# Kernel tuning notes

Measured on AMD Instinct MI355X. Metric: run time of the kernel, lower is better.

The kernel has to match this reference:

```python
import jax, jax.numpy as jnp
import numpy as np

N, T, D, H = 64, 1024, 512, 512

def setup_inputs() -> dict:
    key = jax.random.key(0)
    k1, k2, k3, k4 = jax.random.split(key, 4)
    x = jax.random.normal(k1, (N, T, D), dtype=jnp.float32)
    h0 = jax.random.normal(k2, (N, H), dtype=jnp.float32)
    Wx = jax.random.normal(k3, (D, 4 * H), dtype=jnp.float32) / jnp.sqrt(jnp.float32(D))
    Wh = jax.random.normal(k4, (H, 4 * H), dtype=jnp.float32) / jnp.sqrt(jnp.float32(H))
    b = jnp.zeros((4 * H,), dtype=jnp.float32)
    return {"x": x, "h0": h0, "Wx": Wx, "Wh": Wh, "b": b}

def reference(x, h0, Wx, Wh, b):
    Hd = h0.shape[1]
    c0 = jnp.zeros_like(h0)
    # Input projection for all timesteps at once (same math as per-step x@Wx).
    xw = jnp.einsum('ntd,dk->ntk', x, Wx) + b  # [N, T, 4H]

    def step(carry, xw_t):
        h, c = carry
        a = xw_t + h @ Wh  # [N, 4H]
        i = jax.nn.sigmoid(a[:, 0 * Hd:1 * Hd])
        f = jax.nn.sigmoid(a[:, 1 * Hd:2 * Hd])
        o = jax.nn.sigmoid(a[:, 2 * Hd:3 * Hd])
        g = jnp.tanh(a[:, 3 * Hd:4 * Hd])
        c_next = f * c + i * g
        h_next = o * jnp.tanh(c_next)
        return (h_next, c_next), h_next

    _, hs = jax.lax.scan(step, (h0, c0), jnp.swapaxes(xw, 0, 1))  # hs: [T, N, H]
    return jnp.swapaxes(hs, 0, 1)  # [N, T, H]
```

## Files before the change

kernel.cpp:

```cpp
#include <hip/hip_runtime.h>

typedef _Float16 f16;
typedef _Float16 f16x2 __attribute__((ext_vector_type(2)));
typedef _Float16 f16x8 __attribute__((ext_vector_type(8)));
typedef float f32x4 __attribute__((ext_vector_type(4)));
typedef unsigned int u32;
typedef u32 u32x4 __attribute__((ext_vector_type(4)));

#define OFF_WCAT  67108864L
#define OFF_BP    71303168L
#define OFF_H32   71311360L

constexpr int AS = 536;

__global__ void prep_kernel(const float* __restrict__ x, const float* __restrict__ h0,
                            const float* __restrict__ Wx, const float* __restrict__ Wh,
                            const float* __restrict__ b,
                            f16* __restrict__ x_h, f16* __restrict__ Wcat,
                            float* __restrict__ b_p, u32* __restrict__ h32)
{
    const int tid = blockIdx.x * blockDim.x + threadIdx.x;
    if (tid < 4194304) {
        const float4* src = (const float4*)x;
        float4 a = src[2*tid], c = src[2*tid + 1];
        f16x8 v;
        v[0]=(f16)a.x; v[1]=(f16)a.y; v[2]=(f16)a.z; v[3]=(f16)a.w;
        v[4]=(f16)c.x; v[5]=(f16)c.y; v[6]=(f16)c.z; v[7]=(f16)c.w;
        *(f16x8*)(x_h + (long)tid*8) = v;
    }
    if (tid < 2097152) {
        int q = tid >> 10, k = tid & 1023;
        int u = q >> 2, g = q & 3;
        float v = (k < 512) ? Wx[(long)k*2048 + g*512 + u]
                            : Wh[(long)(k-512)*2048 + g*512 + u];
        Wcat[tid] = (f16)v;
    }
    if (tid < 32768) {
        union { f16 h; unsigned short s; } cv; cv.h = (f16)h0[tid];
        h32[tid]         = (u32)cv.s;
        h32[32768 + tid] = 0xFFFF0000u;
    }
    if (tid < 2048)  b_p[tid] = b[(tid & 3)*512 + (tid >> 2)];
}


__device__ __forceinline__ void ld16_coh(const u32* p, u32x4& a, u32x4& b,
                                         u32x4& c, u32x4& d)
{
    asm volatile("global_load_dwordx4 %0, %4, off sc0 sc1\n\t"
                 "global_load_dwordx4 %1, %5, off sc0 sc1\n\t"
                 "global_load_dwordx4 %2, %6, off sc0 sc1\n\t"
                 "global_load_dwordx4 %3, %7, off sc0 sc1\n\t"
                 "s_waitcnt vmcnt(0)"
                 : "=&v"(a), "=&v"(b), "=&v"(c), "=&v"(d)
                 : "v"(p), "v"(p + 4), "v"(p + 8), "v"(p + 12)
                 : "memory");
}

__device__ __forceinline__ void st_w32(u32* p, unsigned v)
{
    asm volatile("global_store_dword %0, %1, off sc0 sc1" :: "v"(p), "v"(v) : "memory");
}

__device__ __forceinline__ void poll_stage(f16* __restrict__ Ah,
                                           const u32* __restrict__ wbase,
                                           unsigned tgt, int tid)
{
    const u32* p = wbase + tid * 16;
    u32x4 A, B, C, D;
    while (true) {
        ld16_coh(p, A, B, C, D);
        unsigned m;
        m  = (A.x>>16)^tgt; m |= (A.y>>16)^tgt; m |= (A.z>>16)^tgt; m |= (A.w>>16)^tgt;
        m |= (B.x>>16)^tgt; m |= (B.y>>16)^tgt; m |= (B.z>>16)^tgt; m |= (B.w>>16)^tgt;
        m |= (C.x>>16)^tgt; m |= (C.y>>16)^tgt; m |= (C.z>>16)^tgt; m |= (C.w>>16)^tgt;
        m |= (D.x>>16)^tgt; m |= (D.y>>16)^tgt; m |= (D.z>>16)^tgt; m |= (D.w>>16)^tgt;
        if (m == 0) break;
    }
    u32x4 lo, hi;
    lo.x = (A.x & 0xFFFFu) | (A.y << 16); lo.y = (A.z & 0xFFFFu) | (A.w << 16);
    lo.z = (B.x & 0xFFFFu) | (B.y << 16); lo.w = (B.z & 0xFFFFu) | (B.w << 16);
    hi.x = (C.x & 0xFFFFu) | (C.y << 16); hi.y = (C.z & 0xFFFFu) | (C.w << 16);
    hi.z = (D.x & 0xFFFFu) | (D.y << 16); hi.w = (D.z & 0xFFFFu) | (D.w << 16);
    const int row = tid >> 5;
    const int col = (tid & 31) * 16;
    u32* dst = (u32*)(Ah + row * AS + col);
    *(u32x4*)dst       = lo;
    *(u32x4*)(dst + 4) = hi;
}

__device__ __forceinline__ void mfma_quad(const f16* A, int aoff, const f16x8* wf,
                                          f32x4& a0, f32x4& a1, f32x4& a2, f32x4& a3)
{
    #pragma unroll
    for (int kk = 0; kk < 16; kk += 4) {
        f16x8 f0 = *(const f16x8*)(A + aoff + (kk+0) * 32);
        f16x8 f1 = *(const f16x8*)(A + aoff + (kk+1) * 32);
        f16x8 f2 = *(const f16x8*)(A + aoff + (kk+2) * 32);
        f16x8 f3 = *(const f16x8*)(A + aoff + (kk+3) * 32);
        a0 = __builtin_amdgcn_mfma_f32_16x16x32_f16(f0, wf[kk+0], a0, 0, 0, 0);
        a1 = __builtin_amdgcn_mfma_f32_16x16x32_f16(f1, wf[kk+1], a1, 0, 0, 0);
        a2 = __builtin_amdgcn_mfma_f32_16x16x32_f16(f2, wf[kk+2], a2, 0, 0, 0);
        a3 = __builtin_amdgcn_mfma_f32_16x16x32_f16(f3, wf[kk+3], a3, 0, 0, 0);
    }
}

__device__ __forceinline__ void bar_lds()
{
    asm volatile("s_waitcnt lgkmcnt(0)" ::: "memory");
    __builtin_amdgcn_s_barrier();
}

__global__ __launch_bounds__(256, 1) void lstm_kernel(
    const f16* __restrict__ x_h, const f16* __restrict__ Wcat,
    const float* __restrict__ b_p, u32* __restrict__ h32,
    float* __restrict__ out)
{
    __shared__ f16 Ax[8 * AS];
    __shared__ f16 Ah[8 * AS];
    __shared__ float epil[4 * 16 * 20];

    const int blk  = blockIdx.x;
    const int g    = blk & 7;
    const int wgl  = blk >> 3;
    const int n0   = g * 8;
    const int tid  = threadIdx.x;
    const int wave = tid >> 6;
    const int lane = tid & 63;
    const int c    = lane & 15;
    const int kg   = lane >> 4;
    const int ub   = wgl * 16 + wave * 4;
    const int q0   = ub * 4;

    f16x8 wfrag[32];
    {
        const f16* wp = Wcat + (long)(q0 + c) * 1024 + kg * 8;
        #pragma unroll
        for (int kk = 0; kk < 32; ++kk)
            wfrag[kk] = *(const f16x8*)(wp + kk * 32);
    }
    const float bias = b_p[q0 + c];

    const int aoff = (lane & 7) * AS + kg * 8;
    float* ep = epil + wave * 320;
    const int rb = lane >> 4;
    const int er = lane >> 2;
    const int eu = lane & 3;
    float cst = 0.f;
    int cur = 0;

    const int pr0 = tid >> 6, pch = tid & 63;
    const f16* xb0 = x_h + ((long)(n0 + pr0)     * 1024) * 512 + pch * 8;
    const f16* xb1 = x_h + ((long)(n0 + pr0 + 4) * 1024) * 512 + pch * 8;
    f16* axd0 = Ax + pr0       * AS + pch * 8;
    f16* axd1 = Ax + (pr0 + 4) * AS + pch * 8;

    u32* hb0 = h32 + n0 * 512;
    u32* hb1 = h32 + 32768 + n0 * 512;

    *(f16x8*)axd0 = *(const f16x8*)(xb0);
    *(f16x8*)axd1 = *(const f16x8*)(xb1);
    poll_stage(Ah, hb0, 0u, tid);
    __syncthreads();

    f32x4 a0 = {0.f,0.f,0.f,0.f}, a1 = {0.f,0.f,0.f,0.f};
    f32x4 a2 = {0.f,0.f,0.f,0.f}, a3 = {0.f,0.f,0.f,0.f};
    mfma_quad(Ax, aoff, wfrag, a0, a1, a2, a3);

    for (int t = 0; t < 1024; ++t) {
        f16x8 xv0, xv1;
        if (t < 1023) {
            xv0 = *(const f16x8*)(xb0 + (long)(t + 1) * 512);
            xv1 = *(const f16x8*)(xb1 + (long)(t + 1) * 512);
        }

        mfma_quad(Ah, aoff, wfrag + 16, a0, a1, a2, a3);

        #pragma unroll
        for (int j = 0; j < 4; ++j) {
            float av = ((a0[j] + a1[j]) + (a2[j] + a3[j])) + bias;
            ep[(rb * 4 + j) * 20 + c] = av;
        }

        const int nxt = cur ^ 1;
        if (lane < 32) {
            float4 g4 = *(const float4*)(ep + er * 20 + eu * 4);
            float iv = 1.f / (1.f + __expf(-g4.x));
            float fv = 1.f / (1.f + __expf(-g4.y));
            float ov = 1.f / (1.f + __expf(-g4.z));
            float gv = 2.f / (1.f + __expf(-2.f * g4.w)) - 1.f;
            float cn = fv * cst + iv * gv;
            cst = cn;
            float th = 2.f / (1.f + __expf(-2.f * cn)) - 1.f;
            float hval = ov * th;
            const int n = n0 + er;
            const int u = ub + eu;
            out[((long)n * 1024 + t) * 512 + u] = hval;
            if (t < 1023) {
                union { f16 h; unsigned short s; } cv; cv.h = (f16)hval;
                unsigned w = ((unsigned)(t + 1) << 16) | (unsigned)cv.s;
                st_w32((nxt ? hb1 : hb0) + (n - n0) * 512 + u, w);
            }
        }

        if (t < 1023) {
            bar_lds();

            *(f16x8*)axd0 = xv0;
            *(f16x8*)axd1 = xv1;
            bar_lds();

            a0 = (f32x4){0.f,0.f,0.f,0.f}; a1 = (f32x4){0.f,0.f,0.f,0.f};
            a2 = (f32x4){0.f,0.f,0.f,0.f}; a3 = (f32x4){0.f,0.f,0.f,0.f};
            mfma_quad(Ax, aoff, wfrag, a0, a1, a2, a3);

            poll_stage(Ah, nxt ? hb1 : hb0, (unsigned)(t + 1), tid);
            bar_lds();
            cur = nxt;
        }
    }
}

extern "C" void kernel_launch(void* const* d_in, const int* in_sizes, int n_in,
                              void* d_out, int out_size, void* d_ws, size_t ws_size,
                              hipStream_t stream)
{
    const float* x  = (const float*)d_in[0];
    const float* h0 = (const float*)d_in[1];
    const float* Wx = (const float*)d_in[2];
    const float* Wh = (const float*)d_in[3];
    const float* b  = (const float*)d_in[4];
    float* out = (float*)d_out;

    char* ws = (char*)d_ws;
    f16*   x_h  = (f16*)(ws);
    f16*   Wcat = (f16*)(ws + OFF_WCAT);
    float* b_p  = (float*)(ws + OFF_BP);
    u32*   h32  = (u32*)(ws + OFF_H32);

    prep_kernel<<<16384, 256, 0, stream>>>(x, h0, Wx, Wh, b, x_h, Wcat, b_p, h32);
    lstm_kernel<<<256, 256, 0, stream>>>(x_h, Wcat, b_p, h32, out);
}
```

Measured before the change: 2.239 ms.

## Offload input projection to producer waves via tagged ring buffer

Each workgroup grows to 512 threads. The extra four waves become producers that compute the x@Wx projection ahead of time into an 8-deep ring buffer of tagged fp16 values, and a progress array provides back-pressure. The recurrent waves now only do the h@Wh MFMAs per step and read the precomputed input term. The workgroup barrier is replaced with an LDS atomic counter barrier among the consumer waves. This takes the input GEMM and x loads off the serial critical path, but it adds polling traffic, fp16 rounding of the projection, and reliance on all blocks being co-resident.

```diff
diff --git a/kernel.cpp b/kernel.cpp
--- a/kernel.cpp
+++ b/kernel.cpp
@@ -1,7 +1,6 @@
 #include <hip/hip_runtime.h>
 
 typedef _Float16 f16;
-typedef _Float16 f16x2 __attribute__((ext_vector_type(2)));
 typedef _Float16 f16x8 __attribute__((ext_vector_type(8)));
 typedef float f32x4 __attribute__((ext_vector_type(4)));
 typedef unsigned int u32;
@@ -10,14 +9,18 @@
 #define OFF_WCAT  67108864L
 #define OFF_BP    71303168L
 #define OFF_H32   71311360L
+#define OFF_XW    71573504L
+#define OFF_PROG  75767808L
 
 constexpr int AS = 536;
+constexpr int XW_DEPTH = 8;
 
 __global__ void prep_kernel(const float* __restrict__ x, const float* __restrict__ h0,
                             const float* __restrict__ Wx, const float* __restrict__ Wh,
                             const float* __restrict__ b,
                             f16* __restrict__ x_h, f16* __restrict__ Wcat,
-                            float* __restrict__ b_p, u32* __restrict__ h32)
+                            float* __restrict__ b_p, u32* __restrict__ h32,
+                            u32* __restrict__ xw, u32* __restrict__ prog)
 {
     const int tid = blockIdx.x * blockDim.x + threadIdx.x;
     if (tid < 4194304) {
@@ -40,7 +43,9 @@
         h32[tid]         = (u32)cv.s;
         h32[32768 + tid] = 0xFFFF0000u;
     }
+    if (tid < 1048576) xw[tid] = 0u;
     if (tid < 2048)  b_p[tid] = b[(tid & 3)*512 + (tid >> 2)];
+    if (tid < 256)   prog[tid] = 0u;
 }
 
 
@@ -57,9 +62,29 @@
                  : "memory");
 }
 
+__device__ __forceinline__ unsigned ld_flag(const unsigned int* p)
+{
+    unsigned v;
+    asm volatile("global_load_dword %0, %1, off sc0 sc1\n\ts_waitcnt vmcnt(0)"
+                 : "=&v"(v) : "v"(p) : "memory");
+    return v;
+}
+
 __device__ __forceinline__ void st_w32(u32* p, unsigned v)
 {
     asm volatile("global_store_dword %0, %1, off sc0 sc1" :: "v"(p), "v"(v) : "memory");
+}
+
+__device__ __forceinline__ void ld4_nw(const u32* p, u32x4& v)
+{
+    asm volatile("global_load_dwordx4 %0, %1, off sc0 sc1"
+                 : "=&v"(v) : "v"(p) : "memory");
+}
+
+__device__ __forceinline__ float pay(u32 w)
+{
+    union { unsigned short s; f16 h; } u; u.s = (unsigned short)w;
+    return (float)u.h;
 }
 
 __device__ __forceinline__ void poll_stage(f16* __restrict__ Ah,
@@ -105,118 +130,162 @@
     }
 }
 
-__device__ __forceinline__ void bar_lds()
-{
+__device__ __forceinline__ void cbar(unsigned* cnt, unsigned& phase)
+{
+    phase += 4;
     asm volatile("s_waitcnt lgkmcnt(0)" ::: "memory");
-    __builtin_amdgcn_s_barrier();
-}
-
-__global__ __launch_bounds__(256, 1) void lstm_kernel(
+    if ((threadIdx.x & 63) == 0) atomicAdd(cnt, 1u);
+    while (*((volatile unsigned*)cnt) < phase) {}
+    asm volatile("" ::: "memory");
+}
+
+__global__ __launch_bounds__(512, 1) void lstm_kernel(
     const f16* __restrict__ x_h, const f16* __restrict__ Wcat,
     const float* __restrict__ b_p, u32* __restrict__ h32,
-    float* __restrict__ out)
-{
-    __shared__ f16 Ax[8 * AS];
+    u32* __restrict__ xw, u32* __restrict__ prog, float* __restrict__ out)
+{
     __shared__ f16 Ah[8 * AS];
     __shared__ float epil[4 * 16 * 20];
+    __shared__ unsigned rcnt;
 
     const int blk  = blockIdx.x;
-    const int g    = blk & 7;
-    const int wgl  = blk >> 3;
-    const int n0   = g * 8;
     const int tid  = threadIdx.x;
-    const int wave = tid >> 6;
     const int lane = tid & 63;
     const int c    = lane & 15;
     const int kg   = lane >> 4;
-    const int ub   = wgl * 16 + wave * 4;
-    const int q0   = ub * 4;
-
-    f16x8 wfrag[32];
-    {
-        const f16* wp = Wcat + (long)(q0 + c) * 1024 + kg * 8;
-        #pragma unroll
-        for (int kk = 0; kk < 32; ++kk)
-            wfrag[kk] = *(const f16x8*)(wp + kk * 32);
-    }
-    const float bias = b_p[q0 + c];
-
-    const int aoff = (lane & 7) * AS + kg * 8;
-    float* ep = epil + wave * 320;
-    const int rb = lane >> 4;
-    const int er = lane >> 2;
-    const int eu = lane & 3;
-    float cst = 0.f;
-    int cur = 0;
-
-    const int pr0 = tid >> 6, pch = tid & 63;
-    const f16* xb0 = x_h + ((long)(n0 + pr0)     * 1024) * 512 + pch * 8;
-    const f16* xb1 = x_h + ((long)(n0 + pr0 + 4) * 1024) * 512 + pch * 8;
-    f16* axd0 = Ax + pr0       * AS + pch * 8;
-    f16* axd1 = Ax + (pr0 + 4) * AS + pch * 8;
-
-    u32* hb0 = h32 + n0 * 512;
-    u32* hb1 = h32 + 32768 + n0 * 512;
-
-    *(f16x8*)axd0 = *(const f16x8*)(xb0);
-    *(f16x8*)axd1 = *(const f16x8*)(xb1);
-    poll_stage(Ah, hb0, 0u, tid);
+    const int rb   = kg;
+
+    if (tid == 0) rcnt = 0u;
     __syncthreads();
 
-    f32x4 a0 = {0.f,0.f,0.f,0.f}, a1 = {0.f,0.f,0.f,0.f};
-    f32x4 a2 = {0.f,0.f,0.f,0.f}, a3 = {0.f,0.f,0.f,0.f};
-    mfma_quad(Ax, aoff, wfrag, a0, a1, a2, a3);
-
-    for (int t = 0; t < 1024; ++t) {
-        f16x8 xv0, xv1;
-        if (t < 1023) {
-            xv0 = *(const f16x8*)(xb0 + (long)(t + 1) * 512);
-            xv1 = *(const f16x8*)(xb1 + (long)(t + 1) * 512);
+    if (tid < 256) {
+        const int g = blk & 7, wgl = blk >> 3, n0 = g * 8;
+        const int wave = tid >> 6;
+        const int ub = wgl * 16 + wave * 4, q0 = ub * 4;
+
+        f16x8 wfh[16];
+        {
+            const f16* wp = Wcat + (long)(q0 + c) * 1024 + 512 + kg * 8;
+            #pragma unroll
+            for (int kk = 0; kk < 16; ++kk) wfh[kk] = *(const f16x8*)(wp + kk * 32);
         }
-
-        mfma_quad(Ah, aoff, wfrag + 16, a0, a1, a2, a3);
-
-        #pragma unroll
-        for (int j = 0; j < 4; ++j) {
-            float av = ((a0[j] + a1[j]) + (a2[j] + a3[j])) + bias;
-            ep[(rb * 4 + j) * 20 + c] = av;
+        const int aoff = (lane & 7) * AS + kg * 8;
+        float* ep = epil + wave * 320;
+        const int er = lane >> 2, eu = lane & 3;
+        const float4 b4 = *(const float4*)(b_p + q0 + eu * 4);
+        float cst = 0.f;
+
+        u32* hb0 = h32 + n0 * 512;
+        u32* hb1 = h32 + 32768 + n0 * 512;
+        u32* mypr = prog + g * 32 + wgl;
+        const long xwrow = (long)(n0 + er) * 2048 + q0 + eu * 4;
+
+        u32x4 wpre;
+        if (lane < 32) ld4_nw(xw + xwrow, wpre);
+        poll_stage(Ah, hb0, 0u, tid);
+        unsigned phase = 0;
+        cbar(&rcnt, phase);
+
+        for (int t = 0; t < 1024; ++t) {
+            f32x4 a0 = {0.f,0.f,0.f,0.f}, a1 = {0.f,0.f,0.f,0.f};
+            f32x4 a2 = {0.f,0.f,0.f,0.f}, a3 = {0.f,0.f,0.f,0.f};
+            mfma_quad(Ah, aoff, wfh, a0, a1, a2, a3);
+
+            #pragma unroll
+            for (int j = 0; j < 4; ++j)
+                ep[(rb * 4 + j) * 20 + c] = (a0[j] + a1[j]) + (a2[j] + a3[j]);
+
+            if (lane < 32) {
+                float4 g4 = *(const float4*)(ep + er * 20 + eu * 4);
+                u32x4 w = wpre;
+                asm volatile("s_waitcnt vmcnt(0)" : "+v"(w) :: "memory");
+                __builtin_amdgcn_sched_barrier(0);
+                const unsigned want = (unsigned)(t + 1);
+                const u32* xwp = xw + (long)(t & (XW_DEPTH-1)) * 131072 + xwrow;
+                while ((w.x >> 16) != want || (w.y >> 16) != want ||
+                       (w.z >> 16) != want || (w.w >> 16) != want) {
+                    asm volatile("global_load_dwordx4 %0, %1, off sc0 sc1\n\t"
+                                 "s_waitcnt vmcnt(0)"
+                                 : "=&v"(w) : "v"(xwp) : "memory");
+                }
+                g4.x += b4.x + pay(w.x);
+                g4.y += b4.y + pay(w.y);
+                g4.z += b4.z + pay(w.z);
+                g4.w += b4.w + pay(w.w);
+                float iv = 1.f / (1.f + __expf(-g4.x));
+                float fv = 1.f / (1.f + __expf(-g4.y));
+                float ov = 1.f / (1.f + __expf(-g4.z));
+                float gv = 2.f / (1.f + __expf(-2.f * g4.w)) - 1.f;
+                float cn = fv * cst + iv * gv;
+                cst = cn;
+                float th = 2.f / (1.f + __expf(-2.f * cn)) - 1.f;
+                float hval = ov * th;
+                const int n = n0 + er;
+                const int u = ub + eu;
+                out[((long)n * 1024 + t) * 512 + u] = hval;
+                if (t < 1023) {
+                    union { f16 h; unsigned short s; } cv; cv.h = (f16)hval;
+                    unsigned hw = ((unsigned)(t + 1) << 16) | (unsigned)cv.s;
+                    st_w32((((t + 1) & 1) ? hb1 : hb0) + er * 512 + u, hw);
+                }
+            }
+
+            cbar(&rcnt, phase);
+            if (tid == 0) st_w32(mypr, (unsigned)(t + 1));
+
+            if (t < 1023) {
+                if (lane < 32)
+                    ld4_nw(xw + (long)((t + 1) & (XW_DEPTH-1)) * 131072 + xwrow, wpre);
+                poll_stage(Ah, ((t + 1) & 1) ? hb1 : hb0, (unsigned)(t + 1), tid);
+                cbar(&rcnt, phase);
+            }
         }
-
-        const int nxt = cur ^ 1;
-        if (lane < 32) {
-            float4 g4 = *(const float4*)(ep + er * 20 + eu * 4);
-            float iv = 1.f / (1.f + __expf(-g4.x));
-            float fv = 1.f / (1.f + __expf(-g4.y));
-            float ov = 1.f / (1.f + __expf(-g4.z));
-            float gv = 2.f / (1.f + __expf(-2.f * g4.w)) - 1.f;
-            float cn = fv * cst + iv * gv;
-            cst = cn;
-            float th = 2.f / (1.f + __expf(-2.f * cn)) - 1.f;
-            float hval = ov * th;
-            const int n = n0 + er;
-            const int u = ub + eu;
-            out[((long)n * 1024 + t) * 512 + u] = hval;
-            if (t < 1023) {
-                union { f16 h; unsigned short s; } cv; cv.h = (f16)hval;
-                unsigned w = ((unsigned)(t + 1) << 16) | (unsigned)cv.s;
-                st_w32((nxt ? hb1 : hb0) + (n - n0) * 512 + u, w);
-            }
+    } else {
+        const int w    = blk * 4 + (tid >> 6) - 4;
+        const int tile = w & 511;
+        const int par  = w >> 9;
+        const int slab = tile >> 7;
+        const int q0p  = (tile & 127) * 16;
+
+        f16x8 wfx[16];
+        {
+            const f16* wp = Wcat + (long)(q0p + c) * 1024 + kg * 8;
+            #pragma unroll
+            for (int kk = 0; kk < 16; ++kk) wfx[kk] = *(const f16x8*)(wp + kk * 32);
         }
-
-        if (t < 1023) {
-            bar_lds();
-
-            *(f16x8*)axd0 = xv0;
-            *(f16x8*)axd1 = xv1;
-            bar_lds();
-
-            a0 = (f32x4){0.f,0.f,0.f,0.f}; a1 = (f32x4){0.f,0.f,0.f,0.f};
-            a2 = (f32x4){0.f,0.f,0.f,0.f}; a3 = (f32x4){0.f,0.f,0.f,0.f};
-            mfma_quad(Ax, aoff, wfrag, a0, a1, a2, a3);
-
-            poll_stage(Ah, nxt ? hb1 : hb0, (unsigned)(t + 1), tid);
-            bar_lds();
-            cur = nxt;
+        const f16* xa = x_h + ((long)(slab * 16 + c) * 1024) * 512 + kg * 8;
+        const u32* prp = prog + slab * 64 + lane;
+
+        for (int tt = par; tt < 1024; tt += 2) {
+            if (tt >= XW_DEPTH) {
+                while (true) {
+                    unsigned pr = ld_flag(prp);
+                    if (__all((int)pr >= tt - (XW_DEPTH - 1))) break;
+                    __builtin_amdgcn_s_sleep(8);
+                }
+            }
+            const f16* at = xa + (long)tt * 512;
+            f16x8 af[16];
+            #pragma unroll
+            for (int kk = 0; kk < 16; ++kk) af[kk] = *(const f16x8*)(at + kk * 32);
+            f32x4 a0 = {0.f,0.f,0.f,0.f}, a1 = {0.f,0.f,0.f,0.f};
+            f32x4 a2 = {0.f,0.f,0.f,0.f}, a3 = {0.f,0.f,0.f,0.f};
+            #pragma unroll
+            for (int kk = 0; kk < 16; kk += 4) {
+                a0 = __builtin_amdgcn_mfma_f32_16x16x32_f16(af[kk+0], wfx[kk+0], a0, 0, 0, 0);
+                a1 = __builtin_amdgcn_mfma_f32_16x16x32_f16(af[kk+1], wfx[kk+1], a1, 0, 0, 0);
+                a2 = __builtin_amdgcn_mfma_f32_16x16x32_f16(af[kk+2], wfx[kk+2], a2, 0, 0, 0);
+                a3 = __builtin_amdgcn_mfma_f32_16x16x32_f16(af[kk+3], wfx[kk+3], a3, 0, 0, 0);
+            }
+            const unsigned tagw = (unsigned)(tt + 1) << 16;
+            u32* d = xw + (long)(tt & (XW_DEPTH-1)) * 131072
+                        + (long)(slab * 16 + rb * 4) * 2048 + q0p + c;
+            #pragma unroll
+            for (int j = 0; j < 4; ++j) {
+                float v = (a0[j] + a1[j]) + (a2[j] + a3[j]);
+                union { f16 h; unsigned short s; } cv; cv.h = (f16)v;
+                st_w32(d + (long)j * 2048, tagw | (unsigned)cv.s);
+            }
         }
     }
 }
@@ -237,7 +306,9 @@
     f16*   Wcat = (f16*)(ws + OFF_WCAT);
     float* b_p  = (float*)(ws + OFF_BP);
     u32*   h32  = (u32*)(ws + OFF_H32);
-
-    prep_kernel<<<16384, 256, 0, stream>>>(x, h0, Wx, Wh, b, x_h, Wcat, b_p, h32);
-    lstm_kernel<<<256, 256, 0, stream>>>(x_h, Wcat, b_p, h32, out);
-}
+    u32*   xw   = (u32*)(ws + OFF_XW);
+    u32*   prog = (u32*)(ws + OFF_PROG);
+
+    prep_kernel<<<16384, 256, 0, stream>>>(x, h0, Wx, Wh, b, x_h, Wcat, b_p, h32, xw, prog);
+    lstm_kernel<<<256, 512, 0, stream>>>(x_h, Wcat, b_p, h32, xw, prog, out);
+}
```

Result: slower. 6.946 ms (+210.2%).

## Load x fragments into registers and double-buffer h stage to drop barriers

Applied to the files above, without the earlier changes.

The x-projection A operand is now loaded straight from global memory into register fragments, prefetched two steps ahead with ping-pong register sets, instead of being staged through shared memory. The h staging buffer is double-buffered in LDS and the loop is unrolled by two, which removes two of the three per-step block barriers. Bias is added once in the epilogue lanes. This raises register pressure considerably (32 extra f16x8 fragments per lane), which risks spills. The new register x loads are uncoalesced per-lane global reads.

```diff
diff --git a/kernel.cpp b/kernel.cpp
--- a/kernel.cpp
+++ b/kernel.cpp
@@ -1,7 +1,6 @@
 #include <hip/hip_runtime.h>
 
 typedef _Float16 f16;
-typedef _Float16 f16x2 __attribute__((ext_vector_type(2)));
 typedef _Float16 f16x8 __attribute__((ext_vector_type(8)));
 typedef float f32x4 __attribute__((ext_vector_type(4)));
 typedef unsigned int u32;
@@ -105,19 +104,69 @@
     }
 }
 
+__device__ __forceinline__ void mfma_quad_reg(const f16x8* xf, const f16x8* wf,
+                                              f32x4& a0, f32x4& a1, f32x4& a2, f32x4& a3)
+{
+    #pragma unroll
+    for (int kk = 0; kk < 16; kk += 4) {
+        a0 = __builtin_amdgcn_mfma_f32_16x16x32_f16(xf[kk+0], wf[kk+0], a0, 0, 0, 0);
+        a1 = __builtin_amdgcn_mfma_f32_16x16x32_f16(xf[kk+1], wf[kk+1], a1, 0, 0, 0);
+        a2 = __builtin_amdgcn_mfma_f32_16x16x32_f16(xf[kk+2], wf[kk+2], a2, 0, 0, 0);
+        a3 = __builtin_amdgcn_mfma_f32_16x16x32_f16(xf[kk+3], wf[kk+3], a3, 0, 0, 0);
+    }
+}
+
 __device__ __forceinline__ void bar_lds()
 {
     asm volatile("s_waitcnt lgkmcnt(0)" ::: "memory");
     __builtin_amdgcn_s_barrier();
 }
+
+#define LSTM_STEP(T, AH_R, AH_P, HB_N, XN, XR)                                \
+  {                                                                           \
+    mfma_quad(AH_R, aoff, wfh, a0, a1, a2, a3);              \
+    _Pragma("unroll")                                                         \
+    for (int j = 0; j < 4; ++j)                                               \
+        ep[(rb * 4 + j) * 20 + c] = (a0[j] + a1[j]) + (a2[j] + a3[j]);        \
+    if (lane < 32) {                                                          \
+        float4 g4 = *(const float4*)(ep + er * 20 + eu * 4);     \
+        g4.x += b4.x; g4.y += b4.y; g4.z += b4.z; g4.w += b4.w;               \
+        float iv = 1.f / (1.f + __expf(-g4.x));                               \
+        float fv = 1.f / (1.f + __expf(-g4.y));                               \
+        float ov = 1.f / (1.f + __expf(-g4.z));                               \
+        float gv = 2.f / (1.f + __expf(-2.f * g4.w)) - 1.f;         \
+        float cn = fv * cst + iv * gv;                                        \
+        cst = cn;                                                             \
+        float th = 2.f / (1.f + __expf(-2.f * cn)) - 1.f;           \
+        float hval = ov * th;                                                 \
+        out[((long)(n0 + er) * 1024 + (T)) * 512 + ub + eu] = hval;           \
+        if ((T) < 1023) {                                                     \
+            union { f16 h; unsigned short s; } cv; cv.h = (f16)hval;          \
+            unsigned hw = ((unsigned)((T) + 1) << 16) | (unsigned)cv.s;       \
+            st_w32((HB_N) + er * 512 + ub + eu, hw);       \
+        }                                                                     \
+    }                                                                         \
+    if ((T) < 1023) {                                                         \
+        a0 = (f32x4){0.f,0.f,0.f,0.f}; a1 = (f32x4){0.f,0.f,0.f,0.f};         \
+        a2 = (f32x4){0.f,0.f,0.f,0.f}; a3 = (f32x4){0.f,0.f,0.f,0.f};         \
+        mfma_quad_reg(XN, wfx, a0, a1, a2, a3);            \
+        if ((T) < 1022) {                                                     \
+            _Pragma("unroll")                                                 \
+            for (int kk = 0; kk < 16; ++kk)                                   \
+                XR[kk] = *(const f16x8*)(xlb + (long)((T) + 2) * 512 + kk*32);\
+        }                                                                     \
+        poll_stage(AH_P, HB_N, (unsigned)((T) + 1), tid);                     \
+        bar_lds();                                     \
+    }                                                                         \
+  }
 
 __global__ __launch_bounds__(256, 1) void lstm_kernel(
     const f16* __restrict__ x_h, const f16* __restrict__ Wcat,
     const float* __restrict__ b_p, u32* __restrict__ h32,
     float* __restrict__ out)
 {
-    __shared__ f16 Ax[8 * AS];
-    __shared__ f16 Ah[8 * AS];
+    __shared__ f16 Ah0[8 * AS];
+    __shared__ f16 Ah1[8 * AS];
     __shared__ float epil[4 * 16 * 20];
 
     const int blk  = blockIdx.x;
@@ -129,95 +178,47 @@
     const int lane = tid & 63;
     const int c    = lane & 15;
     const int kg   = lane >> 4;
+    const int rb   = kg;
     const int ub   = wgl * 16 + wave * 4;
     const int q0   = ub * 4;
 
-    f16x8 wfrag[32];
+    f16x8 wfx[16], wfh[16];
     {
         const f16* wp = Wcat + (long)(q0 + c) * 1024 + kg * 8;
         #pragma unroll
-        for (int kk = 0; kk < 32; ++kk)
-            wfrag[kk] = *(const f16x8*)(wp + kk * 32);
-    }
-    const float bias = b_p[q0 + c];
+        for (int kk = 0; kk < 16; ++kk) wfx[kk] = *(const f16x8*)(wp + kk * 32);
+        #pragma unroll
+        for (int kk = 0; kk < 16; ++kk) wfh[kk] = *(const f16x8*)(wp + 512 + kk * 32);
+    }
 
     const int aoff = (lane & 7) * AS + kg * 8;
     float* ep = epil + wave * 320;
-    const int rb = lane >> 4;
     const int er = lane >> 2;
     const int eu = lane & 3;
+    const float4 b4 = *(const float4*)(b_p + q0 + eu * 4);
     float cst = 0.f;
-    int cur = 0;
-
-    const int pr0 = tid >> 6, pch = tid & 63;
-    const f16* xb0 = x_h + ((long)(n0 + pr0)     * 1024) * 512 + pch * 8;
-    const f16* xb1 = x_h + ((long)(n0 + pr0 + 4) * 1024) * 512 + pch * 8;
-    f16* axd0 = Ax + pr0       * AS + pch * 8;
-    f16* axd1 = Ax + (pr0 + 4) * AS + pch * 8;
 
     u32* hb0 = h32 + n0 * 512;
     u32* hb1 = h32 + 32768 + n0 * 512;
 
-    *(f16x8*)axd0 = *(const f16x8*)(xb0);
-    *(f16x8*)axd1 = *(const f16x8*)(xb1);
-    poll_stage(Ah, hb0, 0u, tid);
-    __syncthreads();
+    const f16* xlb = x_h + ((long)(n0 + (lane & 7)) * 1024) * 512 + kg * 8;
+
+    f16x8 xA[16], xB[16];
+    #pragma unroll
+    for (int kk = 0; kk < 16; ++kk) xA[kk] = *(const f16x8*)(xlb + kk * 32);
+    #pragma unroll
+    for (int kk = 0; kk < 16; ++kk) xB[kk] = *(const f16x8*)(xlb + 512 + kk * 32);
 
     f32x4 a0 = {0.f,0.f,0.f,0.f}, a1 = {0.f,0.f,0.f,0.f};
     f32x4 a2 = {0.f,0.f,0.f,0.f}, a3 = {0.f,0.f,0.f,0.f};
-    mfma_quad(Ax, aoff, wfrag, a0, a1, a2, a3);
-
-    for (int t = 0; t < 1024; ++t) {
-        f16x8 xv0, xv1;
-        if (t < 1023) {
-            xv0 = *(const f16x8*)(xb0 + (long)(t + 1) * 512);
-            xv1 = *(const f16x8*)(xb1 + (long)(t + 1) * 512);
-        }
-
-        mfma_quad(Ah, aoff, wfrag + 16, a0, a1, a2, a3);
-
-        #pragma unroll
-        for (int j = 0; j < 4; ++j) {
-            float av = ((a0[j] + a1[j]) + (a2[j] + a3[j])) + bias;
-            ep[(rb * 4 + j) * 20 + c] = av;
-        }
-
-        const int nxt = cur ^ 1;
-        if (lane < 32) {
-            float4 g4 = *(const float4*)(ep + er * 20 + eu * 4);
-            float iv = 1.f / (1.f + __expf(-g4.x));
-            float fv = 1.f / (1.f + __expf(-g4.y));
-            float ov = 1.f / (1.f + __expf(-g4.z));
-            float gv = 2.f / (1.f + __expf(-2.f * g4.w)) - 1.f;
-            float cn = fv * cst + iv * gv;
-            cst = cn;
-            float th = 2.f / (1.f + __expf(-2.f * cn)) - 1.f;
-            float hval = ov * th;
-            const int n = n0 + er;
-            const int u = ub + eu;
-            out[((long)n * 1024 + t) * 512 + u] = hval;
-            if (t < 1023) {
-                union { f16 h; unsigned short s; } cv; cv.h = (f16)hval;
-                unsigned w = ((unsigned)(t + 1) << 16) | (unsigned)cv.s;
-                st_w32((nxt ? hb1 : hb0) + (n - n0) * 512 + u, w);
-            }
-        }
-
-        if (t < 1023) {
-            bar_lds();
-
-            *(f16x8*)axd0 = xv0;
-            *(f16x8*)axd1 = xv1;
-            bar_lds();
-
-            a0 = (f32x4){0.f,0.f,0.f,0.f}; a1 = (f32x4){0.f,0.f,0.f,0.f};
-            a2 = (f32x4){0.f,0.f,0.f,0.f}; a3 = (f32x4){0.f,0.f,0.f,0.f};
-            mfma_quad(Ax, aoff, wfrag, a0, a1, a2, a3);
-
-            poll_stage(Ah, nxt ? hb1 : hb0, (unsigned)(t + 1), tid);
-            bar_lds();
-            cur = nxt;
-        }
+    mfma_quad_reg(xA, wfx, a0, a1, a2, a3);
+
+    poll_stage(Ah0, hb0, 0u, tid);
+    bar_lds();
+
+    for (int t = 0; t < 1024; t += 2) {
+        LSTM_STEP(t,     Ah0, Ah1, hb1, xB, xA);
+        LSTM_STEP(t + 1, Ah1, Ah0, hb0, xA, xB);
     }
 }
 
```

New measurement: 3.727 ms. +66.5%, slower.
